# Optimization experiments

Measured on AMD Instinct MI355X. Metric: run time of the kernel, lower is better.

Reference implementation:

```python
import jax, jax.numpy as jnp
import numpy as np

B, S, D, H = 2, 2048, 1024, 16
DH = D // H


def setup_inputs() -> dict:
    key = jax.random.key(0)
    ks = jax.random.split(key, 12)
    std = 0.02
    return {
        "q_in": jax.random.normal(ks[0], (B, S, D), jnp.float32),
        "k_in": jax.random.normal(ks[1], (B, S, D), jnp.float32),
        "v_in": jax.random.normal(ks[2], (B, S, D), jnp.float32),
        "mask": jnp.zeros((B, 1, S, S), jnp.float32),
        "Wq": jax.random.truncated_normal(ks[3], -2., 2., (D, D), jnp.float32) * std,
        "bq": jnp.zeros((D,), jnp.float32),
        "Wk": jax.random.truncated_normal(ks[4], -2., 2., (D, D), jnp.float32) * std,
        "bk": jnp.zeros((D,), jnp.float32),
        "Wv": jax.random.truncated_normal(ks[5], -2., 2., (D, D), jnp.float32) * std,
        "bv": jnp.zeros((D,), jnp.float32),
        "Wo": jax.random.truncated_normal(ks[6], -2., 2., (D, D), jnp.float32) * std,
        "bo": jnp.zeros((D,), jnp.float32),
    }


def reference(q_in, k_in, v_in, mask, Wq, bq, Wk, bk, Wv, bv, Wo, bo):
    # projections: [B,S,D]
    q = q_in @ Wq + bq
    k = k_in @ Wk + bk
    v = v_in @ Wv + bv
    # split heads -> [B,H,S,DH]
    def split(x):
        return x.reshape(B, -1, H, DH).transpose(0, 2, 1, 3)
    q, k, v = split(q), split(k), split(v)
    # scaled dot-product attention (dropout is identity: training=False)
    scale = 1.0 / jnp.sqrt(jnp.float32(DH))
    scores = jnp.einsum("bhqd,bhkd->bhqk", q, k) * scale + mask
    attn = jax.nn.softmax(scores, axis=-1)
    ctx = jnp.einsum("bhqk,bhkd->bhqd", attn, v)
    # merge heads -> [B,S,D]
    ctx = ctx.transpose(0, 2, 1, 3).reshape(B, -1, D)
    out = ctx @ Wo + bo
    return out, attn
```

## Files before the change

kernel.cpp:

```cpp
#include <hip/hip_runtime.h>

#define B_  2
#define S_  2048
#define D_  1024
#define H_  16
#define DH_ 64

typedef _Float16 f16x8 __attribute__((ext_vector_type(8)));
typedef float    f32x4 __attribute__((ext_vector_type(4)));

#define MFMA16(a, b, c) __builtin_amdgcn_mfma_f32_16x16x32_f16((a), (b), (c), 0, 0, 0)

__global__ __launch_bounds__(256) void gemm_qkv(
    const float* __restrict__ q_in, const float* __restrict__ k_in, const float* __restrict__ v_in,
    const float* __restrict__ Wq,  const float* __restrict__ Wk,  const float* __restrict__ Wv,
    const float* __restrict__ bq,  const float* __restrict__ bk,  const float* __restrict__ bv,
    _Float16* __restrict__ Qh, _Float16* __restrict__ Kh, _Float16* __restrict__ Vh)
{
    const int z = blockIdx.z;
    const float* X    = (z == 0) ? q_in : (z == 1) ? k_in : v_in;
    const float* W    = (z == 0) ? Wq   : (z == 1) ? Wk   : Wv;
    const float* bias = (z == 0) ? bq   : (z == 1) ? bk   : bv;
    _Float16*    dst  = (z == 0) ? Qh   : (z == 1) ? Kh   : Vh;

    __shared__ _Float16 As[64][40];
    __shared__ _Float16 Bs[64][40];

    const int tid  = threadIdx.x;
    const int lane = tid & 63, wave = tid >> 6;
    const int quad = lane >> 4, col = lane & 15;
    const int wm = wave >> 1, wn = wave & 1;
    const int bm0 = blockIdx.y * 64, bn0 = blockIdx.x * 64;

    const int ar  = tid >> 2, ac  = (tid & 3) * 8;
    const int bkr = tid >> 3, bn8 = (tid & 7) * 8;

    f32x4 acc[2][2] = {};

    for (int k0 = 0; k0 < D_; k0 += 32) {
        const float* ap = X + (size_t)(bm0 + ar) * D_ + k0 + ac;
        float4 a0 = *(const float4*)ap;
        float4 a1 = *(const float4*)(ap + 4);
        f16x8 av = { (_Float16)a0.x, (_Float16)a0.y, (_Float16)a0.z, (_Float16)a0.w,
                     (_Float16)a1.x, (_Float16)a1.y, (_Float16)a1.z, (_Float16)a1.w };
        *(f16x8*)&As[ar][ac] = av;

        const float* bp = W + (size_t)(k0 + bkr) * D_ + bn0 + bn8;
        float4 b0 = *(const float4*)bp;
        float4 b1 = *(const float4*)(bp + 4);
        Bs[bn8 + 0][bkr] = (_Float16)b0.x;
        Bs[bn8 + 1][bkr] = (_Float16)b0.y;
        Bs[bn8 + 2][bkr] = (_Float16)b0.z;
        Bs[bn8 + 3][bkr] = (_Float16)b0.w;
        Bs[bn8 + 4][bkr] = (_Float16)b1.x;
        Bs[bn8 + 5][bkr] = (_Float16)b1.y;
        Bs[bn8 + 6][bkr] = (_Float16)b1.z;
        Bs[bn8 + 7][bkr] = (_Float16)b1.w;
        __syncthreads();

        f16x8 a[2], b[2];
#pragma unroll
        for (int r = 0; r < 2; ++r) a[r] = *(const f16x8*)&As[wm * 32 + r * 16 + col][quad * 8];
#pragma unroll
        for (int c = 0; c < 2; ++c) b[c] = *(const f16x8*)&Bs[wn * 32 + c * 16 + col][quad * 8];
#pragma unroll
        for (int r = 0; r < 2; ++r)
#pragma unroll
            for (int c = 0; c < 2; ++c)
                acc[r][c] = MFMA16(a[r], b[c], acc[r][c]);
        __syncthreads();
    }

#pragma unroll
    for (int r = 0; r < 2; ++r)
#pragma unroll
        for (int c = 0; c < 2; ++c) {
            const int n = bn0 + wn * 32 + c * 16 + col;
            const int h = n >> 6, dh = n & 63;
            const float bi = bias[n];
#pragma unroll
            for (int e = 0; e < 4; ++e) {
                const int m = bm0 + wm * 32 + r * 16 + quad * 4 + e;
                const int bb = m >> 11, s = m & 2047;
                dst[(((size_t)(bb * H_ + h)) * S_ + s) * DH_ + dh] =
                    (_Float16)(acc[r][c][e] + bi);
            }
        }
}

__global__ __launch_bounds__(256) void attn_kernel(
    const _Float16* __restrict__ Qh, const _Float16* __restrict__ Kh,
    const _Float16* __restrict__ Vh, const float* __restrict__ mask,
    float* __restrict__ attn, _Float16* __restrict__ ctx)
{
    const int bh = blockIdx.y;
    const int b = bh >> 4, h = bh & 15;
    const int qb0 = blockIdx.x * 64;
    const int tid = threadIdx.x, lane = tid & 63, wave = tid >> 6;
    const int quad = lane >> 4, col = lane & 15;

    __shared__ _Float16 Ks[32][72];
    __shared__ _Float16 Vts[64][40];
    __shared__ _Float16 Ps[4][16][40];

    const int qrow0 = qb0 + wave * 16;

    const _Float16* qp = Qh + ((size_t)bh * S_ + qrow0 + col) * DH_;
    const f16x8 aq0 = *(const f16x8*)(qp + quad * 8);
    const f16x8 aq1 = *(const f16x8*)(qp + 32 + quad * 8);

    const float LOG2E = 1.4426950408889634f;
    const float scale_l2 = 0.125f * LOG2E;

    float mrow[4] = { -1e30f, -1e30f, -1e30f, -1e30f };
    float lrow[4] = { 0.f, 0.f, 0.f, 0.f };

    const int krow = tid >> 3, kc8 = (tid & 7) * 8;

    for (int kt = 0; kt < S_; kt += 32) {
        *(f16x8*)&Ks[krow][kc8] =
            *(const f16x8*)(Kh + ((size_t)bh * S_ + kt + krow) * DH_ + kc8);
        __syncthreads();
#pragma unroll
        for (int c = 0; c < 2; ++c) {
            f16x8 b0 = *(const f16x8*)&Ks[c * 16 + col][quad * 8];
            f16x8 b1 = *(const f16x8*)&Ks[c * 16 + col][32 + quad * 8];
            f32x4 sc = {};
            sc = MFMA16(aq0, b0, sc);
            sc = MFMA16(aq1, b1, sc);
#pragma unroll
            for (int e = 0; e < 4; ++e) {
                const int q = qrow0 + quad * 4 + e;
                const float s2 = sc[e] * scale_l2 +
                    mask[((size_t)b * S_ + q) * S_ + kt + c * 16 + col] * LOG2E;
                const float nm = fmaxf(mrow[e], s2);
                lrow[e] = lrow[e] * exp2f(mrow[e] - nm) + exp2f(s2 - nm);
                mrow[e] = nm;
            }
        }
        __syncthreads();
    }

#pragma unroll
    for (int off = 1; off < 16; off <<= 1) {
#pragma unroll
        for (int e = 0; e < 4; ++e) {
            const float om = __shfl_xor(mrow[e], off, 64);
            const float ol = __shfl_xor(lrow[e], off, 64);
            const float nm = fmaxf(mrow[e], om);
            lrow[e] = lrow[e] * exp2f(mrow[e] - nm) + ol * exp2f(om - nm);
            mrow[e] = nm;
        }
    }
    float invl[4];
#pragma unroll
    for (int e = 0; e < 4; ++e) invl[e] = 1.0f / lrow[e];

    f32x4 cacc[4] = {};
    for (int kt = 0; kt < S_; kt += 32) {
        *(f16x8*)&Ks[krow][kc8] =
            *(const f16x8*)(Kh + ((size_t)bh * S_ + kt + krow) * DH_ + kc8);
        {
            f16x8 v0 = *(const f16x8*)(Vh + ((size_t)bh * S_ + kt + krow) * DH_ + kc8);
#pragma unroll
            for (int j = 0; j < 8; ++j) Vts[kc8 + j][krow] = v0[j];
        }
        __syncthreads();

#pragma unroll
        for (int c = 0; c < 2; ++c) {
            f16x8 b0 = *(const f16x8*)&Ks[c * 16 + col][quad * 8];
            f16x8 b1 = *(const f16x8*)&Ks[c * 16 + col][32 + quad * 8];
            f32x4 sc = {};
            sc = MFMA16(aq0, b0, sc);
            sc = MFMA16(aq1, b1, sc);
#pragma unroll
            for (int e = 0; e < 4; ++e) {
                const int q = qrow0 + quad * 4 + e;
                const float s2 = sc[e] * scale_l2 +
                    mask[((size_t)b * S_ + q) * S_ + kt + c * 16 + col] * LOG2E;
                const float p = exp2f(s2 - mrow[e]) * invl[e];
                attn[((size_t)bh * S_ + q) * S_ + kt + c * 16 + col] = p;
                Ps[wave][quad * 4 + e][c * 16 + col] = (_Float16)p;
            }
        }

        {
            f16x8 apf = *(const f16x8*)&Ps[wave][col][quad * 8];
#pragma unroll
            for (int nt = 0; nt < 4; ++nt) {
                f16x8 bv = *(const f16x8*)&Vts[nt * 16 + col][quad * 8];
                cacc[nt] = MFMA16(apf, bv, cacc[nt]);
            }
        }
        __syncthreads();
    }

#pragma unroll
    for (int nt = 0; nt < 4; ++nt)
#pragma unroll
        for (int e = 0; e < 4; ++e) {
            const int s = qrow0 + quad * 4 + e;
            const int d = h * DH_ + nt * 16 + col;
            ctx[((size_t)b * S_ + s) * D_ + d] = (_Float16)cacc[nt][e];
        }
}

__global__ __launch_bounds__(256) void gemm_out(
    const _Float16* __restrict__ X, const float* __restrict__ W,
    const float* __restrict__ bias, float* __restrict__ out)
{
    __shared__ _Float16 As[64][40];
    __shared__ _Float16 Bs[64][40];

    const int tid  = threadIdx.x;
    const int lane = tid & 63, wave = tid >> 6;
    const int quad = lane >> 4, col = lane & 15;
    const int wm = wave >> 1, wn = wave & 1;
    const int bm0 = blockIdx.y * 64, bn0 = blockIdx.x * 64;

    const int ar  = tid >> 2, ac  = (tid & 3) * 8;
    const int bkr = tid >> 3, bn8 = (tid & 7) * 8;

    f32x4 acc[2][2] = {};

    for (int k0 = 0; k0 < D_; k0 += 32) {
        *(f16x8*)&As[ar][ac] = *(const f16x8*)(X + (size_t)(bm0 + ar) * D_ + k0 + ac);

        const float* bp = W + (size_t)(k0 + bkr) * D_ + bn0 + bn8;
        float4 b0 = *(const float4*)bp;
        float4 b1 = *(const float4*)(bp + 4);
        Bs[bn8 + 0][bkr] = (_Float16)b0.x;
        Bs[bn8 + 1][bkr] = (_Float16)b0.y;
        Bs[bn8 + 2][bkr] = (_Float16)b0.z;
        Bs[bn8 + 3][bkr] = (_Float16)b0.w;
        Bs[bn8 + 4][bkr] = (_Float16)b1.x;
        Bs[bn8 + 5][bkr] = (_Float16)b1.y;
        Bs[bn8 + 6][bkr] = (_Float16)b1.z;
        Bs[bn8 + 7][bkr] = (_Float16)b1.w;
        __syncthreads();

        f16x8 a[2], b[2];
#pragma unroll
        for (int r = 0; r < 2; ++r) a[r] = *(const f16x8*)&As[wm * 32 + r * 16 + col][quad * 8];
#pragma unroll
        for (int c = 0; c < 2; ++c) b[c] = *(const f16x8*)&Bs[wn * 32 + c * 16 + col][quad * 8];
#pragma unroll
        for (int r = 0; r < 2; ++r)
#pragma unroll
            for (int c = 0; c < 2; ++c)
                acc[r][c] = MFMA16(a[r], b[c], acc[r][c]);
        __syncthreads();
    }

#pragma unroll
    for (int r = 0; r < 2; ++r)
#pragma unroll
        for (int c = 0; c < 2; ++c) {
            const int n = bn0 + wn * 32 + c * 16 + col;
            const float bi = bias[n];
#pragma unroll
            for (int e = 0; e < 4; ++e) {
                const int m = bm0 + wm * 32 + r * 16 + quad * 4 + e;
                out[(size_t)m * D_ + n] = acc[r][c][e] + bi;
            }
        }
}

extern "C" void kernel_launch(void* const* d_in, const int* in_sizes, int n_in,
                              void* d_out, int out_size, void* d_ws, size_t ws_size,
                              hipStream_t stream) {
    const float* q_in = (const float*)d_in[0];
    const float* k_in = (const float*)d_in[1];
    const float* v_in = (const float*)d_in[2];
    const float* mask = (const float*)d_in[3];
    const float* Wq   = (const float*)d_in[4];
    const float* bq   = (const float*)d_in[5];
    const float* Wk   = (const float*)d_in[6];
    const float* bk   = (const float*)d_in[7];
    const float* Wv   = (const float*)d_in[8];
    const float* bv   = (const float*)d_in[9];
    const float* Wo   = (const float*)d_in[10];
    const float* bo   = (const float*)d_in[11];

    float* out  = (float*)d_out;
    float* attn = out + (size_t)B_ * S_ * D_;

    const size_t elems = (size_t)B_ * H_ * S_ * DH_;
    _Float16* Qh  = (_Float16*)d_ws;
    _Float16* Kh  = Qh + elems;
    _Float16* Vh  = Kh + elems;
    _Float16* Ctx = Vh + elems;

    gemm_qkv<<<dim3(16, 64, 3), 256, 0, stream>>>(q_in, k_in, v_in,
                                                  Wq, Wk, Wv, bq, bk, bv,
                                                  Qh, Kh, Vh);
    attn_kernel<<<dim3(32, 32), 256, 0, stream>>>(Qh, Kh, Vh, mask, attn, Ctx);
    gemm_out<<<dim3(16, 64), 256, 0, stream>>>(Ctx, Wo, bo, out);
}
```

Measured before the change: 1.016 ms.

## Pre-convert inputs and weights to fp16, use 128x128 tiles with direct-to-LDS loads

Adds pre-pass kernels that convert the activations to fp16 and transpose and convert the weights to fp16. The fp16 activations are staged in the attention output buffer as scratch before attention overwrites it. The projection GEMMs then use 128x128 tiles with global_load_lds 16-byte direct-to-LDS loads, replacing per-element fp32 loads, conversion and scattered transposed LDS stores. This trades two extra conversion passes and more registers per thread for cheaper, wider GEMM main loops and more reuse per tile. The shared-memory tiles have no padding, so MFMA fragment reads may hit LDS bank conflicts.

```diff
diff --git a/kernel.cpp b/kernel.cpp
--- a/kernel.cpp
+++ b/kernel.cpp
@@ -11,79 +11,178 @@
 
 #define MFMA16(a, b, c) __builtin_amdgcn_mfma_f32_16x16x32_f16((a), (b), (c), 0, 0, 0)
 
-__global__ __launch_bounds__(256) void gemm_qkv(
-    const float* __restrict__ q_in, const float* __restrict__ k_in, const float* __restrict__ v_in,
-    const float* __restrict__ Wq,  const float* __restrict__ Wk,  const float* __restrict__ Wv,
-    const float* __restrict__ bq,  const float* __restrict__ bk,  const float* __restrict__ bv,
-    _Float16* __restrict__ Qh, _Float16* __restrict__ Kh, _Float16* __restrict__ Vh)
+#define GLD16(gptr, lptr)                                                           \
+    __builtin_amdgcn_global_load_lds(                                               \
+        (const __attribute__((address_space(1))) void*)(gptr),                      \
+        (__attribute__((address_space(3))) void*)(lptr), 16, 0, 0)
+
+__global__ __launch_bounds__(256) void cvt_x(
+    const float* __restrict__ q, const float* __restrict__ k, const float* __restrict__ v,
+    _Float16* __restrict__ x16)
+{
+    const int z = blockIdx.y;
+    const float* src = (z == 0) ? q : (z == 1) ? k : v;
+    _Float16* dst = x16 + (size_t)z * (4096 * 1024);
+    const size_t i = ((size_t)blockIdx.x * 256 + threadIdx.x) * 8;
+    float4 a = *(const float4*)(src + i);
+    float4 b = *(const float4*)(src + i + 4);
+    f16x8 o = { (_Float16)a.x, (_Float16)a.y, (_Float16)a.z, (_Float16)a.w,
+                (_Float16)b.x, (_Float16)b.y, (_Float16)b.z, (_Float16)b.w };
+    *(f16x8*)(dst + i) = o;
+}
+
+__global__ __launch_bounds__(256) void cvt_w(
+    const float* __restrict__ Wq, const float* __restrict__ Wk,
+    const float* __restrict__ Wv, const float* __restrict__ Wo,
+    _Float16* __restrict__ Wt3,
+    _Float16* __restrict__ Wot)
 {
     const int z = blockIdx.z;
-    const float* X    = (z == 0) ? q_in : (z == 1) ? k_in : v_in;
-    const float* W    = (z == 0) ? Wq   : (z == 1) ? Wk   : Wv;
-    const float* bias = (z == 0) ? bq   : (z == 1) ? bk   : bv;
-    _Float16*    dst  = (z == 0) ? Qh   : (z == 1) ? Kh   : Vh;
-
-    __shared__ _Float16 As[64][40];
-    __shared__ _Float16 Bs[64][40];
-
-    const int tid  = threadIdx.x;
-    const int lane = tid & 63, wave = tid >> 6;
+    const float* W = (z == 0) ? Wq : (z == 1) ? Wk : (z == 2) ? Wv : Wo;
+    _Float16* Wt = (z < 3) ? (Wt3 + (size_t)z * (1024 * 1024)) : Wot;
+
+    __shared__ _Float16 T[64][72];
+    const int k0 = blockIdx.y * 64, n0 = blockIdx.x * 64;
+    const int r = threadIdx.x >> 3, c8 = (threadIdx.x & 7) * 8;
+
+#pragma unroll
+    for (int it = 0; it < 2; ++it) {
+        const int row = it * 32 + r;
+        const float* p = W + (size_t)(k0 + row) * D_ + n0 + c8;
+        float4 a = *(const float4*)p;
+        float4 b = *(const float4*)(p + 4);
+        _Float16* t = &T[row][c8];
+        t[0] = (_Float16)a.x; t[1] = (_Float16)a.y; t[2] = (_Float16)a.z; t[3] = (_Float16)a.w;
+        t[4] = (_Float16)b.x; t[5] = (_Float16)b.y; t[6] = (_Float16)b.z; t[7] = (_Float16)b.w;
+    }
+    __syncthreads();
+#pragma unroll
+    for (int it = 0; it < 2; ++it) {
+        const int nrow = it * 32 + r;
+        f16x8 o = { T[c8 + 0][nrow], T[c8 + 1][nrow], T[c8 + 2][nrow], T[c8 + 3][nrow],
+                    T[c8 + 4][nrow], T[c8 + 5][nrow], T[c8 + 6][nrow], T[c8 + 7][nrow] };
+        *(f16x8*)(Wt + (size_t)(n0 + nrow) * D_ + k0 + c8) = o;
+    }
+}
+
+__global__ __launch_bounds__(256) void gemm_qkv_f(
+    const _Float16* __restrict__ X16, const _Float16* __restrict__ Wt3,
+    const float* __restrict__ bq, const float* __restrict__ bk, const float* __restrict__ bv,
+    _Float16* __restrict__ QKVh)
+{
+    const int z = blockIdx.z;
+    const _Float16* Ag = X16 + (size_t)z * (4096 * 1024);
+    const _Float16* Bg = Wt3 + (size_t)z * (1024 * 1024);
+    const float* bias = (z == 0) ? bq : (z == 1) ? bk : bv;
+    _Float16* dst = QKVh + (size_t)z * (4096 * 1024);
+
+    __shared__ _Float16 As[128 * 32];
+    __shared__ _Float16 Bs[128 * 32];
+
+    const int tid = threadIdx.x, lane = tid & 63, wave = tid >> 6;
     const int quad = lane >> 4, col = lane & 15;
     const int wm = wave >> 1, wn = wave & 1;
-    const int bm0 = blockIdx.y * 64, bn0 = blockIdx.x * 64;
-
-    const int ar  = tid >> 2, ac  = (tid & 3) * 8;
-    const int bkr = tid >> 3, bn8 = (tid & 7) * 8;
-
-    f32x4 acc[2][2] = {};
+    const int bm0 = blockIdx.y * 128, bn0 = blockIdx.x * 128;
+
+    const int srow = lane >> 2;
+    const int ska  = (lane & 3) * 8;
+
+    f32x4 acc[4][4] = {};
 
     for (int k0 = 0; k0 < D_; k0 += 32) {
-        const float* ap = X + (size_t)(bm0 + ar) * D_ + k0 + ac;
-        float4 a0 = *(const float4*)ap;
-        float4 a1 = *(const float4*)(ap + 4);
-        f16x8 av = { (_Float16)a0.x, (_Float16)a0.y, (_Float16)a0.z, (_Float16)a0.w,
-                     (_Float16)a1.x, (_Float16)a1.y, (_Float16)a1.z, (_Float16)a1.w };
-        *(f16x8*)&As[ar][ac] = av;
-
-        const float* bp = W + (size_t)(k0 + bkr) * D_ + bn0 + bn8;
-        float4 b0 = *(const float4*)bp;
-        float4 b1 = *(const float4*)(bp + 4);
-        Bs[bn8 + 0][bkr] = (_Float16)b0.x;
-        Bs[bn8 + 1][bkr] = (_Float16)b0.y;
-        Bs[bn8 + 2][bkr] = (_Float16)b0.z;
-        Bs[bn8 + 3][bkr] = (_Float16)b0.w;
-        Bs[bn8 + 4][bkr] = (_Float16)b1.x;
-        Bs[bn8 + 5][bkr] = (_Float16)b1.y;
-        Bs[bn8 + 6][bkr] = (_Float16)b1.z;
-        Bs[bn8 + 7][bkr] = (_Float16)b1.w;
-        __syncthreads();
-
-        f16x8 a[2], b[2];
-#pragma unroll
-        for (int r = 0; r < 2; ++r) a[r] = *(const f16x8*)&As[wm * 32 + r * 16 + col][quad * 8];
-#pragma unroll
-        for (int c = 0; c < 2; ++c) b[c] = *(const f16x8*)&Bs[wn * 32 + c * 16 + col][quad * 8];
-#pragma unroll
-        for (int r = 0; r < 2; ++r)
-#pragma unroll
-            for (int c = 0; c < 2; ++c)
+#pragma unroll
+        for (int i = 0; i < 2; ++i) {
+            const int ch = wave * 2 + i;
+            const int row = ch * 16 + srow;
+            GLD16(Ag + (size_t)(bm0 + row) * D_ + k0 + ska, &As[ch * 512]);
+            GLD16(Bg + (size_t)(bn0 + row) * D_ + k0 + ska, &Bs[ch * 512]);
+        }
+        __syncthreads();
+
+        f16x8 a[4], b[4];
+#pragma unroll
+        for (int r = 0; r < 4; ++r)
+            a[r] = *(const f16x8*)&As[(wm * 64 + r * 16 + col) * 32 + quad * 8];
+#pragma unroll
+        for (int c = 0; c < 4; ++c)
+            b[c] = *(const f16x8*)&Bs[(wn * 64 + c * 16 + col) * 32 + quad * 8];
+#pragma unroll
+        for (int r = 0; r < 4; ++r)
+#pragma unroll
+            for (int c = 0; c < 4; ++c)
                 acc[r][c] = MFMA16(a[r], b[c], acc[r][c]);
         __syncthreads();
     }
 
 #pragma unroll
-    for (int r = 0; r < 2; ++r)
-#pragma unroll
-        for (int c = 0; c < 2; ++c) {
-            const int n = bn0 + wn * 32 + c * 16 + col;
+    for (int r = 0; r < 4; ++r)
+#pragma unroll
+        for (int c = 0; c < 4; ++c) {
+            const int n = bn0 + wn * 64 + c * 16 + col;
             const int h = n >> 6, dh = n & 63;
             const float bi = bias[n];
 #pragma unroll
             for (int e = 0; e < 4; ++e) {
-                const int m = bm0 + wm * 32 + r * 16 + quad * 4 + e;
+                const int m = bm0 + wm * 64 + r * 16 + quad * 4 + e;
                 const int bb = m >> 11, s = m & 2047;
                 dst[(((size_t)(bb * H_ + h)) * S_ + s) * DH_ + dh] =
                     (_Float16)(acc[r][c][e] + bi);
+            }
+        }
+}
+
+__global__ __launch_bounds__(256) void gemm_out_f(
+    const _Float16* __restrict__ Ag, const _Float16* __restrict__ Bg,
+    const float* __restrict__ bias, float* __restrict__ out)
+{
+    __shared__ _Float16 As[128 * 32];
+    __shared__ _Float16 Bs[128 * 32];
+
+    const int tid = threadIdx.x, lane = tid & 63, wave = tid >> 6;
+    const int quad = lane >> 4, col = lane & 15;
+    const int wm = wave >> 1, wn = wave & 1;
+    const int bm0 = blockIdx.y * 128, bn0 = blockIdx.x * 128;
+
+    const int srow = lane >> 2;
+    const int ska  = (lane & 3) * 8;
+
+    f32x4 acc[4][4] = {};
+
+    for (int k0 = 0; k0 < D_; k0 += 32) {
+#pragma unroll
+        for (int i = 0; i < 2; ++i) {
+            const int ch = wave * 2 + i;
+            const int row = ch * 16 + srow;
+            GLD16(Ag + (size_t)(bm0 + row) * D_ + k0 + ska, &As[ch * 512]);
+            GLD16(Bg + (size_t)(bn0 + row) * D_ + k0 + ska, &Bs[ch * 512]);
+        }
+        __syncthreads();
+
+        f16x8 a[4], b[4];
+#pragma unroll
+        for (int r = 0; r < 4; ++r)
+            a[r] = *(const f16x8*)&As[(wm * 64 + r * 16 + col) * 32 + quad * 8];
+#pragma unroll
+        for (int c = 0; c < 4; ++c)
+            b[c] = *(const f16x8*)&Bs[(wn * 64 + c * 16 + col) * 32 + quad * 8];
+#pragma unroll
+        for (int r = 0; r < 4; ++r)
+#pragma unroll
+            for (int c = 0; c < 4; ++c)
+                acc[r][c] = MFMA16(a[r], b[c], acc[r][c]);
+        __syncthreads();
+    }
+
+#pragma unroll
+    for (int r = 0; r < 4; ++r)
+#pragma unroll
+        for (int c = 0; c < 4; ++c) {
+            const int n = bn0 + wn * 64 + c * 16 + col;
+            const float bi = bias[n];
+#pragma unroll
+            for (int e = 0; e < 4; ++e) {
+                const int m = bm0 + wm * 64 + r * 16 + quad * 4 + e;
+                out[(size_t)m * D_ + n] = acc[r][c][e] + bi;
             }
         }
 }
@@ -203,67 +302,6 @@
             const int s = qrow0 + quad * 4 + e;
             const int d = h * DH_ + nt * 16 + col;
             ctx[((size_t)b * S_ + s) * D_ + d] = (_Float16)cacc[nt][e];
-        }
-}
-
-__global__ __launch_bounds__(256) void gemm_out(
-    const _Float16* __restrict__ X, const float* __restrict__ W,
-    const float* __restrict__ bias, float* __restrict__ out)
-{
-    __shared__ _Float16 As[64][40];
-    __shared__ _Float16 Bs[64][40];
-
-    const int tid  = threadIdx.x;
-    const int lane = tid & 63, wave = tid >> 6;
-    const int quad = lane >> 4, col = lane & 15;
-    const int wm = wave >> 1, wn = wave & 1;
-    const int bm0 = blockIdx.y * 64, bn0 = blockIdx.x * 64;
-
-    const int ar  = tid >> 2, ac  = (tid & 3) * 8;
-    const int bkr = tid >> 3, bn8 = (tid & 7) * 8;
-
-    f32x4 acc[2][2] = {};
-
-    for (int k0 = 0; k0 < D_; k0 += 32) {
-        *(f16x8*)&As[ar][ac] = *(const f16x8*)(X + (size_t)(bm0 + ar) * D_ + k0 + ac);
-
-        const float* bp = W + (size_t)(k0 + bkr) * D_ + bn0 + bn8;
-        float4 b0 = *(const float4*)bp;
-        float4 b1 = *(const float4*)(bp + 4);
-        Bs[bn8 + 0][bkr] = (_Float16)b0.x;
-        Bs[bn8 + 1][bkr] = (_Float16)b0.y;
-        Bs[bn8 + 2][bkr] = (_Float16)b0.z;
-        Bs[bn8 + 3][bkr] = (_Float16)b0.w;
-        Bs[bn8 + 4][bkr] = (_Float16)b1.x;
-        Bs[bn8 + 5][bkr] = (_Float16)b1.y;
-        Bs[bn8 + 6][bkr] = (_Float16)b1.z;
-        Bs[bn8 + 7][bkr] = (_Float16)b1.w;
-        __syncthreads();
-
-        f16x8 a[2], b[2];
-#pragma unroll
-        for (int r = 0; r < 2; ++r) a[r] = *(const f16x8*)&As[wm * 32 + r * 16 + col][quad * 8];
-#pragma unroll
-        for (int c = 0; c < 2; ++c) b[c] = *(const f16x8*)&Bs[wn * 32 + c * 16 + col][quad * 8];
-#pragma unroll
-        for (int r = 0; r < 2; ++r)
-#pragma unroll
-            for (int c = 0; c < 2; ++c)
-                acc[r][c] = MFMA16(a[r], b[c], acc[r][c]);
-        __syncthreads();
-    }
-
-#pragma unroll
-    for (int r = 0; r < 2; ++r)
-#pragma unroll
-        for (int c = 0; c < 2; ++c) {
-            const int n = bn0 + wn * 32 + c * 16 + col;
-            const float bi = bias[n];
-#pragma unroll
-            for (int e = 0; e < 4; ++e) {
-                const int m = bm0 + wm * 32 + r * 16 + quad * 4 + e;
-                out[(size_t)m * D_ + n] = acc[r][c][e] + bi;
-            }
         }
 }
 
@@ -287,14 +325,19 @@
     float* attn = out + (size_t)B_ * S_ * D_;
 
     const size_t elems = (size_t)B_ * H_ * S_ * DH_;
+
     _Float16* Qh  = (_Float16*)d_ws;
     _Float16* Kh  = Qh + elems;
     _Float16* Vh  = Kh + elems;
     _Float16* Ctx = Vh + elems;
-
-    gemm_qkv<<<dim3(16, 64, 3), 256, 0, stream>>>(q_in, k_in, v_in,
-                                                  Wq, Wk, Wv, bq, bk, bv,
-                                                  Qh, Kh, Vh);
+    _Float16* Wot = Ctx + elems;
+
+    _Float16* X16 = (_Float16*)attn;
+    _Float16* Wt3 = X16 + 3 * elems;
+
+    cvt_x<<<dim3(2048, 3), 256, 0, stream>>>(q_in, k_in, v_in, X16);
+    cvt_w<<<dim3(16, 16, 4), 256, 0, stream>>>(Wq, Wk, Wv, Wo, Wt3, Wot);
+    gemm_qkv_f<<<dim3(8, 32, 3), 256, 0, stream>>>(X16, Wt3, bq, bk, bv, Qh);
     attn_kernel<<<dim3(32, 32), 256, 0, stream>>>(Qh, Kh, Vh, mask, attn, Ctx);
-    gemm_out<<<dim3(16, 64), 256, 0, stream>>>(Ctx, Wo, bo, out);
-}
+    gemm_out_f<<<dim3(8, 32), 256, 0, stream>>>(Ctx, Wot, bo, out);
+}
```

After: 930.1 us. 1.09x faster.
